# Kernel optimization log

Measured on AMD Instinct MI355X. Metric: run time of the kernel, lower is better.

## Reference

```python
import jax, jax.numpy as jnp
import numpy as np
from jax import lax

B = 32      # point clouds per batch
P = 1024    # points per cloud (equal-sized, contiguous in batch vector)
K = 20      # kNN neighbors (includes self, as in PyG knn)
N = B * P


def _w(key, fan_in, fan_out):
    return jax.random.normal(key, (fan_in, fan_out), dtype=jnp.float32) / np.sqrt(fan_in)


def setup_inputs() -> dict:
    key = jax.random.key(0)
    ks = jax.random.split(key, 12)
    return {
        "pos": jax.random.normal(ks[0], (N, 3), dtype=jnp.float32),
        "batch": jnp.repeat(jnp.arange(B, dtype=jnp.int32), P),
        # conv1 MLP([6,64,64]): Linear(6,64)+BN+ReLU, Linear(64,64) plain
        "conv1_W1": _w(ks[1], 6, 64),
        "conv1_b1": jnp.zeros((64,), jnp.float32),
        "conv1_bn_scale": jnp.ones((64,), jnp.float32),   # BN eval folded affine
        "conv1_bn_bias": jnp.zeros((64,), jnp.float32),
        "conv1_W2": _w(ks[2], 64, 64),
        "conv1_b2": jnp.zeros((64,), jnp.float32),
        # conv2 MLP([128,128]): single plain Linear(128,128)
        "conv2_W": _w(ks[3], 128, 128),
        "conv2_b": jnp.zeros((128,), jnp.float32),
        # lin: Linear(64+128, 128)
        "lin_W": _w(ks[4], 192, 128),
        "lin_b": jnp.zeros((128,), jnp.float32),
    }


def _edge_conv(x, mlp_fn):
    # x: [B, P, d]. Dynamic kNN in feature space per cloud, edge MLP, max-aggregate.
    sq = jnp.sum(x * x, axis=-1)                                  # [B,P]
    dist = sq[:, :, None] - 2.0 * jnp.einsum('bpd,bqd->bpq', x, x) + sq[:, None, :]
    _, idx = lax.top_k(-dist, K)                                  # [B,P,K] nearest (incl. self)
    x_j = jax.vmap(lambda xb, ib: xb[ib])(x, idx)                 # [B,P,K,d] gather neighbors
    x_i = jnp.broadcast_to(x[:, :, None, :], x_j.shape)
    e = jnp.concatenate([x_i, x_j - x_i], axis=-1)                # [B,P,K,2d]
    return jnp.max(mlp_fn(e), axis=2)                             # max aggregation -> [B,P,out]


def reference(pos, batch, conv1_W1, conv1_b1, conv1_bn_scale, conv1_bn_bias,
              conv1_W2, conv1_b2, conv2_W, conv2_b, lin_W, lin_b):
    x = pos.reshape(B, P, 3)

    def mlp1(e):
        h = e @ conv1_W1 + conv1_b1
        h = jax.nn.relu(h * conv1_bn_scale + conv1_bn_bias)       # BN(eval) + ReLU
        return h @ conv1_W2 + conv1_b2                            # plain last layer

    def mlp2(e):
        return e @ conv2_W + conv2_b                              # plain single layer

    x1 = _edge_conv(x, mlp1)                                      # [B,P,64]
    x2 = _edge_conv(x1, mlp2)                                     # [B,P,128]
    h = jnp.concatenate([x1, x2], axis=-1) @ lin_W + lin_b        # [B,P,128]
    # global_max_pool over each cloud via batch ids
    out = jax.ops.segment_max(h.reshape(N, 128), batch, num_segments=B)
    return out                                                    # [B,128]
```

## Files before the change

### kernel.cpp

```cpp
#include <hip/hip_runtime.h>
#include <math.h>

#define NPTS 32768
#define NB 32
#define PP 1024
#define KK 20

using bf16x8 = __attribute__((ext_vector_type(8))) short;
using f32x4 = __attribute__((ext_vector_type(4))) float;

constexpr size_t OFF_X1 = 0;
constexpr size_t OFF_IDX = OFF_X1 + (size_t)NPTS * 64 * 4;
constexpr size_t OFF_U = OFF_IDX + (size_t)NPTS * KK * 4;
constexpr size_t OFF_V = OFF_U + (size_t)NPTS * 128 * 4;
constexpr size_t OFF_X2 = OFF_V + (size_t)NPTS * 128 * 4;
constexpr size_t OFF_H = OFF_X2 + (size_t)NPTS * 128 * 4;
constexpr size_t OFF_PART = OFF_H + (size_t)NPTS * 128 * 4;
constexpr size_t OFF_SQN = OFF_PART + (size_t)32 * 8 * 128 * 4;

__device__ __forceinline__ void topk_insert(unsigned (&l)[KK], unsigned key) {
#pragma unroll
  for (int j = KK - 1; j >= 1; --j) {
    unsigned r;
    asm("v_med3_u32 %0, %1, %2, %3" : "=v"(r) : "v"(key), "v"(l[j - 1]), "v"(l[j]));
    l[j] = r;
  }
  l[0] = key < l[0] ? key : l[0];
}

__device__ __forceinline__ unsigned pack_key(float dist, int q) {
  return (__float_as_uint(dist) & 0xFFFFFC00u) | (unsigned)q;
}

__device__ __forceinline__ void split_bf16(float x, short& hi, short& lo) {
  unsigned u = __float_as_uint(x);
  hi = (short)(u >> 16);
  float fh = __uint_as_float(u & 0xFFFF0000u);
  float r = x - fh;
  lo = (short)(__float_as_uint(r) >> 16);
}

template <int S>
__global__ __launch_bounds__(256, 4) void knn_topk3(const float* __restrict__ x,
                                                    unsigned* __restrict__ pk) {
  constexpr int CH = PP / S;
  __shared__ __align__(16) float xs[1024];
  __shared__ __align__(16) float ys[1024];
  __shared__ __align__(16) float zs[1024];
  int bx = blockIdx.x;
  int s = bx % S;
  int tile = (bx / S) % (PP / 256);
  int b = bx / (S * (PP / 256));
  int tid = threadIdx.x;
  const float* xb = x + (size_t)b * PP * 3;

  for (int t = tid; t < 768; t += 256) {
    float4 v = ((const float4*)xb)[t];
    int e = 4 * t;
    float vals[4] = {v.x, v.y, v.z, v.w};
#pragma unroll
    for (int j = 0; j < 4; ++j) {
      int p = (e + j) / 3, d = (e + j) % 3;
      if (d == 0) xs[p] = vals[j];
      else if (d == 1) ys[p] = vals[j];
      else zs[p] = vals[j];
    }
  }
  __syncthreads();

  int i = tile * 256 + tid;
  float xi0 = xs[i], xi1 = ys[i], xi2 = zs[i];

  unsigned la[KK], lb[KK];
#pragma unroll
  for (int j = 0; j < KK; ++j) { la[j] = 0xFFFFFFFFu; lb[j] = 0xFFFFFFFFu; }

  int q0 = s * CH;
  float4 qx = *(const float4*)&xs[q0];
  float4 qy = *(const float4*)&ys[q0];
  float4 qz = *(const float4*)&zs[q0];
  for (int c = 0; c < CH; c += 4) {
    int qm = (q0 + c + 4) & 1023;
    float4 nqx = *(const float4*)&xs[qm];
    float4 nqy = *(const float4*)&ys[qm];
    float4 nqz = *(const float4*)&zs[qm];
    float cx[4] = {qx.x, qx.y, qx.z, qx.w};
    float cy[4] = {qy.x, qy.y, qy.z, qy.w};
    float cz[4] = {qz.x, qz.y, qz.z, qz.w};
    {
      float d0 = xi0 - cx[0], d1 = xi1 - cy[0], d2 = xi2 - cz[0];
      topk_insert(la, pack_key(fmaf(d0, d0, fmaf(d1, d1, d2 * d2)), q0 + c + 0));
    }
    {
      float d0 = xi0 - cx[2], d1 = xi1 - cy[2], d2 = xi2 - cz[2];
      topk_insert(lb, pack_key(fmaf(d0, d0, fmaf(d1, d1, d2 * d2)), q0 + c + 2));
    }
    {
      float d0 = xi0 - cx[1], d1 = xi1 - cy[1], d2 = xi2 - cz[1];
      topk_insert(la, pack_key(fmaf(d0, d0, fmaf(d1, d1, d2 * d2)), q0 + c + 1));
    }
    {
      float d0 = xi0 - cx[3], d1 = xi1 - cy[3], d2 = xi2 - cz[3];
      topk_insert(lb, pack_key(fmaf(d0, d0, fmaf(d1, d1, d2 * d2)), q0 + c + 3));
    }
    qx = nqx; qy = nqy; qz = nqz;
  }
  size_t base = ((size_t)b * PP + i) * (2 * S) + s * 2;
#pragma unroll
  for (int j = 0; j < KK; ++j) pk[base * KK + j] = la[j];
#pragma unroll
  for (int j = 0; j < KK; ++j) pk[(base + 1) * KK + j] = lb[j];
}

template <int S>
__global__ __launch_bounds__(256) void knn_merge(const unsigned* __restrict__ pk,
                                                 int* __restrict__ idx_out) {
  int p = blockIdx.x * 256 + threadIdx.x;
  const unsigned* g = pk + (size_t)p * S * KK;
  unsigned l[KK];
#pragma unroll
  for (int j = 0; j < KK; ++j) l[j] = g[j];
  for (int s = 1; s < S; ++s) {
    const unsigned* gs = g + s * KK;
    for (int j = 0; j < KK; ++j) {
      unsigned key = gs[j];
      if (key >= l[KK - 1]) break;
      topk_insert(l, key);
    }
  }
#pragma unroll
  for (int j = 0; j < KK; ++j) idx_out[(size_t)p * KK + j] = (int)(l[j] & 1023u);
}

__global__ __launch_bounds__(256) void precompute1(const float* __restrict__ pos,
                                                   const float* __restrict__ W1,
                                                   const float* __restrict__ b1,
                                                   float* __restrict__ u1,
                                                   float* __restrict__ v1) {
  int gid = blockIdx.x * 256 + threadIdx.x;
  int i = gid >> 6, c = gid & 63;
  float p0 = pos[(size_t)i * 3 + 0], p1 = pos[(size_t)i * 3 + 1], p2 = pos[(size_t)i * 3 + 2];
  float a0 = W1[0 * 64 + c], a1 = W1[1 * 64 + c], a2 = W1[2 * 64 + c];
  float g0 = W1[3 * 64 + c], g1 = W1[4 * 64 + c], g2 = W1[5 * 64 + c];
  float v = fmaf(p0, g0, fmaf(p1, g1, p2 * g2));
  float u = b1[c];
  u = fmaf(p0, a0 - g0, u);
  u = fmaf(p1, a1 - g1, u);
  u = fmaf(p2, a2 - g2, u);
  u1[gid] = u;
  v1[gid] = v;
}

__global__ __launch_bounds__(256) void edge_conv1_mfma(
    const float* __restrict__ u1, const float* __restrict__ v1,
    const int* __restrict__ idx, const float* __restrict__ W2,
    const float* __restrict__ scale, const float* __restrict__ bias,
    const float* __restrict__ b2,
    short* __restrict__ x1hl, float* __restrict__ sqn) {
  __shared__ float Cs[160 * 68];
  __shared__ int jt[160];
  __shared__ float xs[512];
  int tid = threadIdx.x;
  int p0 = blockIdx.x * 8;
  int b = p0 >> 10;
  if (tid < 160) {
    int e = tid;
    int i = p0 + e / 20;
    jt[e] = (b << 10) + idx[(size_t)i * KK + e % 20];
  }
  int w = tid >> 6, l = tid & 63, quad = l >> 4, lm = l & 15;
  int kq = quad * 8;
  float4 s00 = *(const float4*)(scale + kq);
  float4 s01 = *(const float4*)(scale + kq + 4);
  float4 s10 = *(const float4*)(scale + 32 + kq);
  float4 s11 = *(const float4*)(scale + 32 + kq + 4);
  float4 c00 = *(const float4*)(bias + kq);
  float4 c01 = *(const float4*)(bias + kq + 4);
  float4 c10 = *(const float4*)(bias + 32 + kq);
  float4 c11 = *(const float4*)(bias + 32 + kq + 4);
  bf16x8 Bh[4][2], Bl[4][2];
#pragma unroll
  for (int nt = 0; nt < 4; ++nt) {
#pragma unroll
    for (int ks = 0; ks < 2; ++ks) {
#pragma unroll
      for (int jj = 0; jj < 8; ++jj) {
        float wv = W2[(size_t)(ks * 32 + kq + jj) * 64 + nt * 16 + lm];
        short hi, lo;
        split_bf16(wv, hi, lo);
        Bh[nt][ks][jj] = hi;
        Bl[nt][ks][jj] = lo;
      }
    }
  }
  __syncthreads();

  for (int s = w; s < 10; s += 4) {
    f32x4 acc[4];
#pragma unroll
    for (int nt = 0; nt < 4; ++nt) acc[nt] = (f32x4){0.f, 0.f, 0.f, 0.f};
    int e = s * 16 + lm;
    int p = e / 20;
    int jrow = jt[e];
    const float* urow = u1 + (size_t)(p0 + p) * 64;
    const float* vrow = v1 + (size_t)jrow * 64;
#pragma unroll
    for (int ks = 0; ks < 2; ++ks) {
      int koff = ks * 32 + kq;
      float4 va = *(const float4*)(vrow + koff);
      float4 vb = *(const float4*)(vrow + koff + 4);
      float4 ua = *(const float4*)(urow + koff);
      float4 ub = *(const float4*)(urow + koff + 4);
      float4 sA = ks ? s10 : s00, sB = ks ? s11 : s01;
      float4 cA = ks ? c10 : c00, cB = ks ? c11 : c01;
      float hv[8];
      hv[0] = fmaxf(fmaf(ua.x + va.x, sA.x, cA.x), 0.f);
      hv[1] = fmaxf(fmaf(ua.y + va.y, sA.y, cA.y), 0.f);
      hv[2] = fmaxf(fmaf(ua.z + va.z, sA.z, cA.z), 0.f);
      hv[3] = fmaxf(fmaf(ua.w + va.w, sA.w, cA.w), 0.f);
      hv[4] = fmaxf(fmaf(ub.x + vb.x, sB.x, cB.x), 0.f);
      hv[5] = fmaxf(fmaf(ub.y + vb.y, sB.y, cB.y), 0.f);
      hv[6] = fmaxf(fmaf(ub.z + vb.z, sB.z, cB.z), 0.f);
      hv[7] = fmaxf(fmaf(ub.w + vb.w, sB.w, cB.w), 0.f);
      bf16x8 Ah, Al;
#pragma unroll
      for (int jj = 0; jj < 8; ++jj) {
        short hi, lo;
        split_bf16(hv[jj], hi, lo);
        Ah[jj] = hi;
        Al[jj] = lo;
      }
#pragma unroll
      for (int nt = 0; nt < 4; ++nt) {
        acc[nt] = __builtin_amdgcn_mfma_f32_16x16x32_bf16(Ah, Bh[nt][ks], acc[nt], 0, 0, 0);
        acc[nt] = __builtin_amdgcn_mfma_f32_16x16x32_bf16(Al, Bh[nt][ks], acc[nt], 0, 0, 0);
        acc[nt] = __builtin_amdgcn_mfma_f32_16x16x32_bf16(Ah, Bl[nt][ks], acc[nt], 0, 0, 0);
      }
    }
#pragma unroll
    for (int nt = 0; nt < 4; ++nt) {
#pragma unroll
      for (int r = 0; r < 4; ++r) {
        Cs[(size_t)(s * 16 + quad * 4 + r) * 68 + nt * 16 + lm] = acc[nt][r];
      }
    }
  }
  __syncthreads();
  for (int o = tid; o < 512; o += 256) {
    int p = o >> 6, c = o & 63;
    float m = -__builtin_inff();
    for (int k = 0; k < KK; ++k) m = fmaxf(m, Cs[(size_t)(p * 20 + k) * 68 + c]);
    m += b2[c];
    size_t gi = (size_t)(p0 + p) * 128 + c;
    short hi, lo;
    split_bf16(m, hi, lo);
    x1hl[gi] = hi;
    x1hl[gi + 64] = lo;
    xs[o] = m;
  }
  __syncthreads();
  if (tid < 8) {
    float ss = 0.f;
    for (int c = 0; c < 64; ++c) {
      float v = xs[tid * 64 + c];
      ss = fmaf(v, v, ss);
    }
    sqn[p0 + tid] = ss;
  }
}

__global__ __launch_bounds__(256, 4) void knn2_mfma(const short* __restrict__ x1hl,
                                                    const float* __restrict__ sqn,
                                                    unsigned* __restrict__ pk) {
  constexpr int TS = 72;
  __shared__ float sqs[512];
  __shared__ __align__(16) short tileH[128 * TS];
  __shared__ __align__(16) short tileL[128 * TS];
  int bx = blockIdx.x;
  int s = bx & 1;
  int pb = bx >> 1;
  int p0 = pb * 64;
  int b = p0 >> 10;
  int tid = threadIdx.x;
  for (int t = tid; t < 512; t += 256) sqs[t] = sqn[(size_t)b * PP + s * 512 + t];
  int w = tid >> 6, l = tid & 63, quad = l >> 4, lm = l & 15;
  size_t gi = (size_t)p0 + w * 16 + lm;
  const short* brow = x1hl + gi * 128 + quad * 8;
  bf16x8 Bh0 = *(const bf16x8*)(brow);
  bf16x8 Bl0 = *(const bf16x8*)(brow + 64);
  bf16x8 Bh1 = *(const bf16x8*)(brow + 32);
  bf16x8 Bl1 = *(const bf16x8*)(brow + 96);
  float sqi = sqn[gi];

  unsigned la[KK], lc[KK];
#pragma unroll
  for (int j = 0; j < KK; ++j) { la[j] = 0xFFFFFFFFu; lc[j] = 0xFFFFFFFFu; }

  int rr = tid & 127, hh = tid >> 7;
  short* dstT = (hh ? tileL : tileH) + rr * TS;
  const size_t cbase = (size_t)b * PP + s * 512;
  const short* srcbase = x1hl + (cbase + rr) * 128 + hh * 64;

  for (int tile = 0; tile < 4; ++tile) {
    __syncthreads();
    {
      const short* src = srcbase + (size_t)tile * 128 * 128;
#pragma unroll
      for (int j = 0; j < 8; ++j)
        *(bf16x8*)(dstT + j * 8) = *(const bf16x8*)(src + j * 8);
    }
    __syncthreads();
#pragma unroll
    for (int it = 0; it < 8; ++it) {
      int row = it * 16 + lm;
      const short* aH = tileH + row * TS + quad * 8;
      const short* aL = tileL + row * TS + quad * 8;
      bf16x8 Ah0 = *(const bf16x8*)(aH);
      bf16x8 Ah1 = *(const bf16x8*)(aH + 32);
      bf16x8 Al0 = *(const bf16x8*)(aL);
      bf16x8 Al1 = *(const bf16x8*)(aL + 32);

      f32x4 acc = (f32x4){0.f, 0.f, 0.f, 0.f};
      acc = __builtin_amdgcn_mfma_f32_16x16x32_bf16(Ah0, Bh0, acc, 0, 0, 0);
      acc = __builtin_amdgcn_mfma_f32_16x16x32_bf16(Al0, Bh0, acc, 0, 0, 0);
      acc = __builtin_amdgcn_mfma_f32_16x16x32_bf16(Ah0, Bl0, acc, 0, 0, 0);
      acc = __builtin_amdgcn_mfma_f32_16x16x32_bf16(Ah1, Bh1, acc, 0, 0, 0);
      acc = __builtin_amdgcn_mfma_f32_16x16x32_bf16(Al1, Bh1, acc, 0, 0, 0);
      acc = __builtin_amdgcn_mfma_f32_16x16x32_bf16(Ah1, Bl1, acc, 0, 0, 0);

      int qloc = tile * 128 + it * 16 + quad * 4;
      int qg = s * 512 + qloc;
      float d0 = fmaxf(0.f, fmaf(-2.f, acc[0], sqi + sqs[qloc + 0]));
      float d2 = fmaxf(0.f, fmaf(-2.f, acc[2], sqi + sqs[qloc + 2]));
      topk_insert(la, pack_key(d0, qg + 0));
      topk_insert(lc, pack_key(d2, qg + 2));
      float d1 = fmaxf(0.f, fmaf(-2.f, acc[1], sqi + sqs[qloc + 1]));
      float d3 = fmaxf(0.f, fmaf(-2.f, acc[3], sqi + sqs[qloc + 3]));
      topk_insert(la, pack_key(d1, qg + 1));
      topk_insert(lc, pack_key(d3, qg + 3));
    }
  }
  unsigned sub = (unsigned)(s * 4 + quad) * 2;
  unsigned* dst = pk + ((size_t)gi * 16 + sub) * KK;
#pragma unroll
  for (int j = 0; j < KK; ++j) dst[j] = la[j];
#pragma unroll
  for (int j = 0; j < KK; ++j) dst[KK + j] = lc[j];
}

__global__ __launch_bounds__(256) void pre2_mfma(const short* __restrict__ x1hl,
                                                 const float* __restrict__ cW,
                                                 const float* __restrict__ cb,
                                                 float* __restrict__ u2,
                                                 float* __restrict__ v2) {
  constexpr int BS = 72;
  __shared__ short Bh[128 * BS];
  __shared__ short Bl[128 * BS];
  int tid = threadIdx.x;
  int nh = blockIdx.x & 1;
  int p0 = (blockIdx.x >> 1) * 64;
  for (int t = tid; t < 64 * 128; t += 256) {
    int k = t >> 7, n = t & 127;
    float wb_ = cW[(size_t)(64 + k) * 128 + n];
    float wv = nh ? wb_ : (cW[(size_t)k * 128 + n] - wb_);
    short hi, lo;
    split_bf16(wv, hi, lo);
    Bh[n * BS + k] = hi;
    Bl[n * BS + k] = lo;
  }
  __syncthreads();
  int w = tid >> 6, l = tid & 63, quad = l >> 4, lm = l & 15;
  int row = p0 + w * 16 + lm;
  f32x4 acc[8];
#pragma unroll
  for (int nt = 0; nt < 8; ++nt) acc[nt] = (f32x4){0.f, 0.f, 0.f, 0.f};
#pragma unroll
  for (int ks = 0; ks < 2; ++ks) {
    int kb = ks * 32 + quad * 8;
    bf16x8 Ah = *(const bf16x8*)(x1hl + (size_t)row * 128 + kb);
    bf16x8 Al = *(const bf16x8*)(x1hl + (size_t)row * 128 + 64 + kb);
#pragma unroll
    for (int nt = 0; nt < 8; ++nt) {
      bf16x8 Wh = *(const bf16x8*)(Bh + (nt * 16 + lm) * BS + kb);
      bf16x8 Wl = *(const bf16x8*)(Bl + (nt * 16 + lm) * BS + kb);
      acc[nt] = __builtin_amdgcn_mfma_f32_16x16x32_bf16(Ah, Wh, acc[nt], 0, 0, 0);
      acc[nt] = __builtin_amdgcn_mfma_f32_16x16x32_bf16(Al, Wh, acc[nt], 0, 0, 0);
      acc[nt] = __builtin_amdgcn_mfma_f32_16x16x32_bf16(Ah, Wl, acc[nt], 0, 0, 0);
    }
  }
  float* out = nh ? v2 : u2;
  int prow = p0 + w * 16 + quad * 4;
#pragma unroll
  for (int nt = 0; nt < 8; ++nt) {
    int col = nt * 16 + lm;
    float bias = nh ? 0.f : cb[col];
#pragma unroll
    for (int r = 0; r < 4; ++r)
      out[(size_t)(prow + r) * 128 + col] = acc[nt][r] + bias;
  }
}

__global__ __launch_bounds__(256) void gathermax2(const float* __restrict__ u2,
                                                  const float* __restrict__ v2,
                                                  const int* __restrict__ idx,
                                                  short* __restrict__ x2hl) {
  int gid = blockIdx.x * 256 + threadIdx.x;
  int i = gid >> 7, c = gid & 127;
  int b = i >> 10;
  const int* myidx = idx + (size_t)i * KK;
  float m = -__builtin_inff();
  for (int k = 0; k < KK; ++k) {
    int j = (b << 10) + myidx[k];
    m = fmaxf(m, v2[(size_t)j * 128 + c]);
  }
  float x = u2[gid] + m;
  short hi, lo;
  split_bf16(x, hi, lo);
  x2hl[(size_t)i * 256 + c] = hi;
  x2hl[(size_t)i * 256 + 128 + c] = lo;
}

__global__ __launch_bounds__(256) void lin_mfma(const short* __restrict__ x1hl,
                                                const short* __restrict__ x2hl,
                                                const float* __restrict__ LW,
                                                const float* __restrict__ lb,
                                                float* __restrict__ h) {
  constexpr int BS = 200;
  __shared__ short Bh[64 * BS];
  __shared__ short Bl[64 * BS];
  int tid = threadIdx.x;
  int nh = blockIdx.x & 1;
  int p0 = (blockIdx.x >> 1) * 64;
  for (int t = tid; t < 192 * 64; t += 256) {
    int k = t >> 6, n = t & 63;
    float wv = LW[(size_t)k * 128 + nh * 64 + n];
    short hi, lo;
    split_bf16(wv, hi, lo);
    Bh[n * BS + k] = hi;
    Bl[n * BS + k] = lo;
  }
  __syncthreads();
  int w = tid >> 6, l = tid & 63, quad = l >> 4, lm = l & 15;
  int row = p0 + w * 16 + lm;
  f32x4 acc[4];
#pragma unroll
  for (int nt = 0; nt < 4; ++nt) acc[nt] = (f32x4){0.f, 0.f, 0.f, 0.f};
#pragma unroll
  for (int ks = 0; ks < 6; ++ks) {
    int kb = ks * 32 + quad * 8;
    bf16x8 Ah, Al;
    if (ks < 2) {
      Ah = *(const bf16x8*)(x1hl + (size_t)row * 128 + kb);
      Al = *(const bf16x8*)(x1hl + (size_t)row * 128 + 64 + kb);
    } else {
      Ah = *(const bf16x8*)(x2hl + (size_t)row * 256 + (kb - 64));
      Al = *(const bf16x8*)(x2hl + (size_t)row * 256 + 128 + (kb - 64));
    }
#pragma unroll
    for (int nt = 0; nt < 4; ++nt) {
      bf16x8 Wh = *(const bf16x8*)(Bh + (nt * 16 + lm) * BS + kb);
      bf16x8 Wl = *(const bf16x8*)(Bl + (nt * 16 + lm) * BS + kb);
      acc[nt] = __builtin_amdgcn_mfma_f32_16x16x32_bf16(Ah, Wh, acc[nt], 0, 0, 0);
      acc[nt] = __builtin_amdgcn_mfma_f32_16x16x32_bf16(Al, Wh, acc[nt], 0, 0, 0);
      acc[nt] = __builtin_amdgcn_mfma_f32_16x16x32_bf16(Ah, Wl, acc[nt], 0, 0, 0);
    }
  }
  int prow = p0 + w * 16 + quad * 4;
#pragma unroll
  for (int nt = 0; nt < 4; ++nt) {
    int col = nh * 64 + nt * 16 + lm;
    float bias = lb[col];
#pragma unroll
    for (int r = 0; r < 4; ++r)
      h[(size_t)(prow + r) * 128 + col] = acc[nt][r] + bias;
  }
}

__global__ __launch_bounds__(128) void segmax_a(const float* __restrict__ h,
                                                float* __restrict__ part) {
  int b = blockIdx.x >> 3, chunk = blockIdx.x & 7;
  int c = threadIdx.x;
  float m = -__builtin_inff();
  for (int p = 0; p < 128; ++p) {
    size_t i = (size_t)b * PP + chunk * 128 + p;
    m = fmaxf(m, h[i * 128 + c]);
  }
  part[(size_t)blockIdx.x * 128 + c] = m;
}

__global__ __launch_bounds__(128) void segmax_b(const float* __restrict__ part,
                                                float* __restrict__ out) {
  int b = blockIdx.x;
  int c = threadIdx.x;
  float m = -__builtin_inff();
  for (int k = 0; k < 8; ++k) m = fmaxf(m, part[((size_t)b * 8 + k) * 128 + c]);
  out[(size_t)b * 128 + c] = m;
}

extern "C" void kernel_launch(void* const* d_in, const int* in_sizes, int n_in,
                              void* d_out, int out_size, void* d_ws, size_t ws_size,
                              hipStream_t stream) {
  const float* pos = (const float*)d_in[0];
  const float* W1 = (const float*)d_in[2];
  const float* b1 = (const float*)d_in[3];
  const float* bn_s = (const float*)d_in[4];
  const float* bn_b = (const float*)d_in[5];
  const float* W2 = (const float*)d_in[6];
  const float* b2 = (const float*)d_in[7];
  const float* cW = (const float*)d_in[8];
  const float* cb = (const float*)d_in[9];
  const float* LW = (const float*)d_in[10];
  const float* lb = (const float*)d_in[11];
  float* out = (float*)d_out;

  char* ws = (char*)d_ws;
  short* x1hl = (short*)(ws + OFF_X1);
  int* idx = (int*)(ws + OFF_IDX);
  float* u1 = (float*)(ws + OFF_U);
  float* v1 = (float*)(ws + OFF_V);
  float* u2 = (float*)(ws + OFF_U);
  float* v2 = (float*)(ws + OFF_V);
  short* x2hl = (short*)(ws + OFF_X2);
  float* hbuf = (float*)(ws + OFF_H);
  float* part = (float*)(ws + OFF_PART);
  float* sqn = (float*)(ws + OFF_SQN);
  unsigned* pk = (unsigned*)(ws + OFF_U);

  knn_topk3<8><<<NB * 4 * 8, 256, 0, stream>>>(pos, pk);
  knn_merge<16><<<NPTS / 256, 256, 0, stream>>>(pk, idx);
  precompute1<<<NPTS * 64 / 256, 256, 0, stream>>>(pos, W1, b1, u1, v1);
  edge_conv1_mfma<<<NPTS / 8, 256, 0, stream>>>(u1, v1, idx, W2, bn_s, bn_b, b2,
                                                x1hl, sqn);
  knn2_mfma<<<NPTS / 64 * 2, 256, 0, stream>>>(x1hl, sqn, pk);
  knn_merge<16><<<NPTS / 256, 256, 0, stream>>>(pk, idx);
  pre2_mfma<<<NPTS / 64 * 2, 256, 0, stream>>>(x1hl, cW, cb, u2, v2);
  gathermax2<<<NPTS * 128 / 256, 256, 0, stream>>>(u2, v2, idx, x2hl);
  lin_mfma<<<NPTS / 64 * 2, 256, 0, stream>>>(x1hl, x2hl, LW, lb, hbuf);
  segmax_a<<<NB * 8, 128, 0, stream>>>(hbuf, part);
  segmax_b<<<NB, 128, 0, stream>>>(part, out);
}
```

Before: 377.0 us.

## Use single top-k list in knn1, double-buffer knn2 tiles, halve merge width

The first kNN kernel now keeps one top-20 list per thread instead of two interleaved lists, so it writes half as many partial lists. The second kNN kernel double-buffers 64-row LDS tiles and prefetches the next tile into registers while MFMA and top-k run on the current one. It also merges its two per-lane lists in-kernel before writing. The merge kernels then read 8 partial lists instead of 16, cutting global traffic and merge work. The cost is a longer serial dependency chain in the knn1 insertion loop and some extra LDS and register use in knn2.

```diff
diff --git a/kernel.cpp b/kernel.cpp
--- a/kernel.cpp
+++ b/kernel.cpp
@@ -71,9 +71,9 @@
   int i = tile * 256 + tid;
   float xi0 = xs[i], xi1 = ys[i], xi2 = zs[i];
 
-  unsigned la[KK], lb[KK];
-#pragma unroll
-  for (int j = 0; j < KK; ++j) { la[j] = 0xFFFFFFFFu; lb[j] = 0xFFFFFFFFu; }
+  unsigned l[KK];
+#pragma unroll
+  for (int j = 0; j < KK; ++j) l[j] = 0xFFFFFFFFu;
 
   int q0 = s * CH;
   float4 qx = *(const float4*)&xs[q0];
@@ -87,29 +87,17 @@
     float cx[4] = {qx.x, qx.y, qx.z, qx.w};
     float cy[4] = {qy.x, qy.y, qy.z, qy.w};
     float cz[4] = {qz.x, qz.y, qz.z, qz.w};
-    {
-      float d0 = xi0 - cx[0], d1 = xi1 - cy[0], d2 = xi2 - cz[0];
-      topk_insert(la, pack_key(fmaf(d0, d0, fmaf(d1, d1, d2 * d2)), q0 + c + 0));
-    }
-    {
-      float d0 = xi0 - cx[2], d1 = xi1 - cy[2], d2 = xi2 - cz[2];
-      topk_insert(lb, pack_key(fmaf(d0, d0, fmaf(d1, d1, d2 * d2)), q0 + c + 2));
-    }
-    {
-      float d0 = xi0 - cx[1], d1 = xi1 - cy[1], d2 = xi2 - cz[1];
-      topk_insert(la, pack_key(fmaf(d0, d0, fmaf(d1, d1, d2 * d2)), q0 + c + 1));
-    }
-    {
-      float d0 = xi0 - cx[3], d1 = xi1 - cy[3], d2 = xi2 - cz[3];
-      topk_insert(lb, pack_key(fmaf(d0, d0, fmaf(d1, d1, d2 * d2)), q0 + c + 3));
+#pragma unroll
+    for (int j = 0; j < 4; ++j) {
+      float d0 = xi0 - cx[j], d1 = xi1 - cy[j], d2 = xi2 - cz[j];
+      float dist = fmaf(d0, d0, fmaf(d1, d1, d2 * d2));
+      topk_insert(l, pack_key(dist, q0 + c + j));
     }
     qx = nqx; qy = nqy; qz = nqz;
   }
-  size_t base = ((size_t)b * PP + i) * (2 * S) + s * 2;
-#pragma unroll
-  for (int j = 0; j < KK; ++j) pk[base * KK + j] = la[j];
-#pragma unroll
-  for (int j = 0; j < KK; ++j) pk[(base + 1) * KK + j] = lb[j];
+  size_t base = ((size_t)b * PP + i) * S + s;
+#pragma unroll
+  for (int j = 0; j < KK; ++j) pk[base * KK + j] = l[j];
 }
 
 template <int S>
@@ -274,8 +262,8 @@
                                                     unsigned* __restrict__ pk) {
   constexpr int TS = 72;
   __shared__ float sqs[512];
-  __shared__ __align__(16) short tileH[128 * TS];
-  __shared__ __align__(16) short tileL[128 * TS];
+  __shared__ __align__(16) short tileH[2][64 * TS];
+  __shared__ __align__(16) short tileL[2][64 * TS];
   int bx = blockIdx.x;
   int s = bx & 1;
   int pb = bx >> 1;
@@ -296,25 +284,36 @@
 #pragma unroll
   for (int j = 0; j < KK; ++j) { la[j] = 0xFFFFFFFFu; lc[j] = 0xFFFFFFFFu; }
 
-  int rr = tid & 127, hh = tid >> 7;
-  short* dstT = (hh ? tileL : tileH) + rr * TS;
-  const size_t cbase = (size_t)b * PP + s * 512;
-  const short* srcbase = x1hl + (cbase + rr) * 128 + hh * 64;
-
-  for (int tile = 0; tile < 4; ++tile) {
-    __syncthreads();
-    {
-      const short* src = srcbase + (size_t)tile * 128 * 128;
-#pragma unroll
-      for (int j = 0; j < 8; ++j)
-        *(bf16x8*)(dstT + j * 8) = *(const bf16x8*)(src + j * 8);
-    }
-    __syncthreads();
-#pragma unroll
-    for (int it = 0; it < 8; ++it) {
+  int rr = tid & 63, seg = tid >> 6;
+  const short* srcbase = x1hl + ((size_t)b * PP + s * 512 + rr) * 128 + seg * 32;
+  {
+    bf16x8 r0 = *(const bf16x8*)(srcbase);
+    bf16x8 r1 = *(const bf16x8*)(srcbase + 8);
+    bf16x8 r2 = *(const bf16x8*)(srcbase + 16);
+    bf16x8 r3 = *(const bf16x8*)(srcbase + 24);
+    short* dst = ((seg < 2) ? tileH[0] : tileL[0]) + rr * TS + (seg & 1) * 32;
+    *(bf16x8*)(dst) = r0;
+    *(bf16x8*)(dst + 8) = r1;
+    *(bf16x8*)(dst + 16) = r2;
+    *(bf16x8*)(dst + 24) = r3;
+  }
+  __syncthreads();
+
+  for (int tile = 0; tile < 8; ++tile) {
+    int buf = tile & 1;
+    bf16x8 r0, r1, r2, r3;
+    if (tile < 7) {
+      const short* src = srcbase + (size_t)(tile + 1) * 64 * 128;
+      r0 = *(const bf16x8*)(src);
+      r1 = *(const bf16x8*)(src + 8);
+      r2 = *(const bf16x8*)(src + 16);
+      r3 = *(const bf16x8*)(src + 24);
+    }
+#pragma unroll
+    for (int it = 0; it < 4; ++it) {
       int row = it * 16 + lm;
-      const short* aH = tileH + row * TS + quad * 8;
-      const short* aL = tileL + row * TS + quad * 8;
+      const short* aH = tileH[buf] + row * TS + quad * 8;
+      const short* aL = tileL[buf] + row * TS + quad * 8;
       bf16x8 Ah0 = *(const bf16x8*)(aH);
       bf16x8 Ah1 = *(const bf16x8*)(aH + 32);
       bf16x8 Al0 = *(const bf16x8*)(aL);
@@ -328,7 +327,7 @@
       acc = __builtin_amdgcn_mfma_f32_16x16x32_bf16(Al1, Bh1, acc, 0, 0, 0);
       acc = __builtin_amdgcn_mfma_f32_16x16x32_bf16(Ah1, Bl1, acc, 0, 0, 0);
 
-      int qloc = tile * 128 + it * 16 + quad * 4;
+      int qloc = tile * 64 + it * 16 + quad * 4;
       int qg = s * 512 + qloc;
       float d0 = fmaxf(0.f, fmaf(-2.f, acc[0], sqi + sqs[qloc + 0]));
       float d2 = fmaxf(0.f, fmaf(-2.f, acc[2], sqi + sqs[qloc + 2]));
@@ -339,13 +338,25 @@
       topk_insert(la, pack_key(d1, qg + 1));
       topk_insert(lc, pack_key(d3, qg + 3));
     }
-  }
-  unsigned sub = (unsigned)(s * 4 + quad) * 2;
-  unsigned* dst = pk + ((size_t)gi * 16 + sub) * KK;
+    if (tile < 7) {
+      __syncthreads();
+      short* dst = ((seg < 2) ? tileH[buf ^ 1] : tileL[buf ^ 1]) + rr * TS + (seg & 1) * 32;
+      *(bf16x8*)(dst) = r0;
+      *(bf16x8*)(dst + 8) = r1;
+      *(bf16x8*)(dst + 16) = r2;
+      *(bf16x8*)(dst + 24) = r3;
+      __syncthreads();
+    }
+  }
+  for (int j = 0; j < KK; ++j) {
+    unsigned key = lc[j];
+    if (key >= la[KK - 1]) break;
+    topk_insert(la, key);
+  }
+  unsigned sub = (unsigned)(s * 4 + quad);
+  unsigned* dst = pk + ((size_t)gi * 8 + sub) * KK;
 #pragma unroll
   for (int j = 0; j < KK; ++j) dst[j] = la[j];
-#pragma unroll
-  for (int j = 0; j < KK; ++j) dst[KK + j] = lc[j];
 }
 
 __global__ __launch_bounds__(256) void pre2_mfma(const short* __restrict__ x1hl,
@@ -527,12 +538,12 @@
   unsigned* pk = (unsigned*)(ws + OFF_U);
 
   knn_topk3<8><<<NB * 4 * 8, 256, 0, stream>>>(pos, pk);
-  knn_merge<16><<<NPTS / 256, 256, 0, stream>>>(pk, idx);
+  knn_merge<8><<<NPTS / 256, 256, 0, stream>>>(pk, idx);
   precompute1<<<NPTS * 64 / 256, 256, 0, stream>>>(pos, W1, b1, u1, v1);
   edge_conv1_mfma<<<NPTS / 8, 256, 0, stream>>>(u1, v1, idx, W2, bn_s, bn_b, b2,
                                                 x1hl, sqn);
   knn2_mfma<<<NPTS / 64 * 2, 256, 0, stream>>>(x1hl, sqn, pk);
-  knn_merge<16><<<NPTS / 256, 256, 0, stream>>>(pk, idx);
+  knn_merge<8><<<NPTS / 256, 256, 0, stream>>>(pk, idx);
   pre2_mfma<<<NPTS / 64 * 2, 256, 0, stream>>>(x1hl, cW, cb, u2, v2);
   gathermax2<<<NPTS * 128 / 256, 256, 0, stream>>>(u2, v2, idx, x2hl);
   lin_mfma<<<NPTS / 64 * 2, 256, 0, stream>>>(x1hl, x2hl, LW, lb, hbuf);
```

After: 341.5 us. 9.4% less time.
